# Kernel optimization log

Measured on AMD Instinct MI355X. Metric: run time of the kernel, lower is better.

Reference implementation:

```python
import jax, jax.numpy as jnp
import numpy as np

N = 100000   # nodes
IN = 128     # in_size
OUT = 64     # out_size (== out_size * layer_num_heads, heads=1)
P = 3        # meta-paths
E = 1600000  # edges per meta-path graph
HID = 32     # semantic attention hidden size


def setup_inputs() -> dict:
    key = jax.random.key(0)
    ks = jax.random.split(key, 8)
    h = jax.random.normal(ks[0], (N, IN), dtype=jnp.float32)
    edge_src = jax.random.randint(ks[1], (P, E), 0, N)
    edge_dst = jax.random.randint(ks[2], (P, E), 0, N)
    # xavier_uniform-style init for linear weights
    def xavier(k, shape):
        fan_in, fan_out = shape[0], shape[1]
        lim = np.sqrt(6.0 / (fan_in + fan_out)).astype(np.float32)
        return jax.random.uniform(k, shape, jnp.float32, -lim, lim)
    gc_w = xavier(ks[3], (IN, OUT))
    gc_b = jnp.zeros((OUT,), jnp.float32)
    sa_w1 = xavier(ks[4], (OUT, HID))
    sa_b1 = jnp.zeros((HID,), jnp.float32)
    sa_w2 = xavier(ks[5], (HID, 1))
    return {"h": h, "gc_w": gc_w, "gc_b": gc_b, "sa_w1": sa_w1,
            "sa_b1": sa_b1, "sa_w2": sa_w2,
            "edge_src": edge_src, "edge_dst": edge_dst}


def _graph_conv(h, gc_w, gc_b, src, dst):
    # DGL GraphConv, norm='both', activation=relu, allow_zero_in_degree.
    ones = jnp.ones(src.shape, h.dtype)
    out_deg = jax.ops.segment_sum(ones, src, num_segments=N)
    in_deg = jax.ops.segment_sum(ones, dst, num_segments=N)
    norm_src = jax.lax.rsqrt(jnp.maximum(out_deg, 1.0))  # [N]
    norm_dst = jax.lax.rsqrt(jnp.maximum(in_deg, 1.0))   # [N]
    # in_feats > out_feats: project first, then aggregate
    feat = (h * norm_src[:, None]) @ gc_w                # [N, OUT]
    agg = jax.ops.segment_sum(feat[src], dst, num_segments=N)  # [N, OUT]
    return jax.nn.relu(agg * norm_dst[:, None] + gc_b)


def reference(h, gc_w, gc_b, sa_w1, sa_b1, sa_w2, edge_src, edge_dst):
    # shared GraphConv applied to each meta-path graph (dropout p=0 -> identity)
    embs = [_graph_conv(h, gc_w, gc_b, edge_src[p], edge_dst[p]) for p in range(P)]
    z = jnp.stack(embs, axis=1)                          # [N, P, OUT]
    # semantic attention: small MLP -> mean over nodes -> softmax over meta-paths
    w = jnp.tanh(z @ sa_w1 + sa_b1) @ sa_w2              # [N, P, 1]
    beta = jax.nn.softmax(w.mean(axis=0), axis=0)        # [P, 1]
    out = (beta[None, :, :] * z).sum(axis=1)             # [N, OUT]
    return out, z
```

## Files before the change

kernel.cpp:

```cpp
#include <hip/hip_runtime.h>

#define NN 100000
#define IN_F 128
#define OUT_F 64
#define PP 3
#define EE 1600000
#define TOT (PP * EE)
#define HID 32
#define SEG_N (PP * NN)
#define NC1024 98
#define NCB (NC1024 * PP)
#define CAPC 19456
#define CAPS 21504
#define CHUNK 8192
#define NSX ((EE + CHUNK - 1) / CHUNK)
#define LCAP 64
#define NFB (NCB * 32)
#define WSLOTS 256

__device__ __forceinline__ unsigned short f2bf(float f) {
    unsigned u = __float_as_uint(f);
    u += 0x7FFFu + ((u >> 16) & 1u);
    return (unsigned short)(u >> 16);
}
__device__ __forceinline__ float bf2f(unsigned short b) {
    return __uint_as_float((unsigned)b << 16);
}
__device__ __forceinline__ float tanh_fast(float x) {
    float ax = fabsf(x);
    float e = __expf(-2.f * ax);
    float t = (1.f - e) / (1.f + e);
    return copysignf(t, x);
}

__global__ void scatter_coarse(const int* __restrict__ src, const int* __restrict__ dst,
                               unsigned* __restrict__ gcur_d, unsigned* __restrict__ gcur_s,
                               unsigned* __restrict__ gbuf_d, unsigned short* __restrict__ gbuf_s) {
    __shared__ unsigned cnt_d[4][NC1024], cnt_s[4][NC1024];
    __shared__ unsigned base_d[NC1024], base_s[NC1024];
    int tid = threadIdx.x;
    int wv = tid >> 6;
    int p = blockIdx.y;
    for (int i = tid; i < 4 * NC1024; i += 256) { cnt_d[i / NC1024][i % NC1024] = 0u; cnt_s[i / NC1024][i % NC1024] = 0u; }
    __syncthreads();
    int e0 = blockIdx.x * CHUNK;
    const int* sp = src + (size_t)p * EE;
    const int* dp = dst + (size_t)p * EE;
    for (int i = 0; i < CHUNK / 256; ++i) {
        int e = e0 + i * 256 + tid;
        if (e < EE) {
            atomicAdd(&cnt_d[wv][dp[e] >> 10], 1u);
            atomicAdd(&cnt_s[wv][sp[e] >> 10], 1u);
        }
    }
    __syncthreads();
    for (int i = tid; i < NC1024; i += 256) {
        unsigned c0 = cnt_d[0][i], c1 = cnt_d[1][i], c2 = cnt_d[2][i], c3 = cnt_d[3][i];
        unsigned tt = c0 + c1 + c2 + c3;
        unsigned base = tt ? atomicAdd(&gcur_d[i * PP + p], (tt + 15u) & ~15u) : 0u;
        base_d[i] = base;
        cnt_d[0][i] = base; cnt_d[1][i] = base + c0;
        cnt_d[2][i] = base + c0 + c1; cnt_d[3][i] = base + c0 + c1 + c2;
        c0 = cnt_s[0][i]; c1 = cnt_s[1][i]; c2 = cnt_s[2][i]; c3 = cnt_s[3][i];
        tt = c0 + c1 + c2 + c3;
        base = tt ? atomicAdd(&gcur_s[i * PP + p], (tt + 31u) & ~31u) : 0u;
        base_s[i] = base;
        cnt_s[0][i] = base; cnt_s[1][i] = base + c0;
        cnt_s[2][i] = base + c0 + c1; cnt_s[3][i] = base + c0 + c1 + c2;
    }
    __syncthreads();
    for (int i = 0; i < CHUNK / 256; ++i) {
        int e = e0 + i * 256 + tid;
        if (e < EE) {
            int s = sp[e], d = dp[e];
            unsigned pd = atomicAdd(&cnt_d[wv][d >> 10], 1u);
            unsigned ps = atomicAdd(&cnt_s[wv][s >> 10], 1u);
            if (pd < CAPC) gbuf_d[(size_t)((d >> 10) * PP + p) * CAPC + pd] = (unsigned)s | ((unsigned)(d & 1023) << 17);
            if (ps < CAPS) gbuf_s[(size_t)((s >> 10) * PP + p) * CAPS + ps] = (unsigned short)(s & 1023);
        }
    }
    __syncthreads();
    for (int i = tid; i < NC1024; i += 256) {
        unsigned base = base_d[i];
        unsigned tt = cnt_d[3][i] - base;
        unsigned padded = (tt + 15u) & ~15u;
        for (unsigned k = tt; k < padded; ++k)
            if (base + k < CAPC) gbuf_d[(size_t)(i * PP + p) * CAPC + base + k] = 0xFFFFFFFFu;
        base = base_s[i];
        tt = cnt_s[3][i] - base;
        padded = (tt + 31u) & ~31u;
        for (unsigned k = tt; k < padded; ++k)
            if (base + k < CAPS) gbuf_s[(size_t)(i * PP + p) * CAPS + base + k] = 0xFFFFu;
    }
}

__global__ void src_hist(const unsigned* __restrict__ gcur_s, const unsigned short* __restrict__ gbuf_s,
                         float* __restrict__ nsrc) {
    __shared__ unsigned hist[4][1024];
    int tid = threadIdx.x;
    int wv = tid >> 6;
    for (int i = tid; i < 4 * 1024; i += 256) hist[i >> 10][i & 1023] = 0u;
    __syncthreads();
    int c = blockIdx.x;
    int blk = c / PP, p = c - blk * PP;
    unsigned cnt = gcur_s[c]; if (cnt > CAPS) cnt = CAPS;
    const unsigned short* gb = gbuf_s + (size_t)c * CAPS;
    for (unsigned j = tid; j < cnt; j += 256) {
        unsigned v = gb[j];
        if (v <= 1023u) atomicAdd(&hist[wv][v], 1u);
    }
    __syncthreads();
    for (int i = tid; i < 1024; i += 256) {
        int n = blk * 1024 + i;
        unsigned hv = hist[0][i] + hist[1][i] + hist[2][i] + hist[3][i];
        if (n < NN) nsrc[p * NN + n] = rsqrtf(fmaxf((float)hv, 1.f));
    }
}

__global__ void __launch_bounds__(256) proj_fused(const float* __restrict__ h,
                                                  const float* __restrict__ gc_w,
                                                  const float* __restrict__ nsrc,
                                                  unsigned short* __restrict__ t0,
                                                  unsigned short* __restrict__ t1,
                                                  unsigned short* __restrict__ t2) {
    __shared__ float w_lds[IN_F * OUT_F];
    __shared__ float h_lds[32 * IN_F];
    int tid = threadIdx.x;
    for (int i = tid; i < IN_F * OUT_F / 4; i += 256)
        ((float4*)w_lds)[i] = ((const float4*)gc_w)[i];
    size_t r0 = (size_t)blockIdx.x * 32;
    for (int i = tid; i < 32 * IN_F / 4; i += 256)
        ((float4*)h_lds)[i] = ((const float4*)(h + r0 * IN_F))[i];
    __syncthreads();
    int wave = tid >> 6, lane = tid & 63;
    float acc[8] = {0.f, 0.f, 0.f, 0.f, 0.f, 0.f, 0.f, 0.f};
    for (int k = 0; k < IN_F; k += 4) {
        float w0 = w_lds[k * OUT_F + lane];
        float w1 = w_lds[(k + 1) * OUT_F + lane];
        float w2 = w_lds[(k + 2) * OUT_F + lane];
        float w3 = w_lds[(k + 3) * OUT_F + lane];
#pragma unroll
        for (int r = 0; r < 8; ++r) {
            float4 hv = *(const float4*)&h_lds[(wave * 8 + r) * IN_F + k];
            acc[r] = fmaf(hv.x, w0, fmaf(hv.y, w1, fmaf(hv.z, w2, fmaf(hv.w, w3, acc[r]))));
        }
    }
#pragma unroll
    for (int r = 0; r < 8; ++r) {
        size_t n = r0 + wave * 8 + r;
        float a = acc[r];
        t0[n * OUT_F + lane] = f2bf(a * nsrc[n]);
        t1[n * OUT_F + lane] = f2bf(a * nsrc[NN + n]);
        t2[n * OUT_F + lane] = f2bf(a * nsrc[2 * NN + n]);
    }
}

__global__ void fine_split(const unsigned* __restrict__ gcur_d, unsigned* __restrict__ gbuf_d,
                           unsigned* __restrict__ foff, unsigned* __restrict__ fcnt) {
    __shared__ unsigned stage[CAPC];
    __shared__ unsigned hist[4][32], pre[32], cur[4][32];
    int c = blockIdx.x;
    int tid = threadIdx.x;
    int wv = tid >> 6;
    if (tid < 32) { hist[0][tid] = 0u; hist[1][tid] = 0u; hist[2][tid] = 0u; hist[3][tid] = 0u; }
    __syncthreads();
    unsigned cnt = gcur_d[c]; if (cnt > CAPC) cnt = CAPC;
    unsigned* gb = gbuf_d + (size_t)c * CAPC;
    for (unsigned j = tid; j < cnt; j += 256) {
        unsigned v = gb[j];
        stage[j] = v;
        if (v != 0xFFFFFFFFu) atomicAdd(&hist[wv][v >> 22], 1u);
    }
    __syncthreads();
    if (tid == 0) {
        unsigned a = 0;
        for (int i = 0; i < 32; ++i) {
            pre[i] = a;
            a += hist[0][i] + hist[1][i] + hist[2][i] + hist[3][i];
        }
    }
    __syncthreads();
    if (tid < 32) {
        unsigned a = pre[tid];
        cur[0][tid] = a; a += hist[0][tid];
        cur[1][tid] = a; a += hist[1][tid];
        cur[2][tid] = a; a += hist[2][tid];
        cur[3][tid] = a; a += hist[3][tid];
        foff[c * 32 + tid] = (unsigned)c * CAPC + pre[tid];
        fcnt[c * 32 + tid] = a - pre[tid];
    }
    __syncthreads();
    for (unsigned j = tid; j < cnt; j += 256) {
        unsigned v = stage[j];
        if (v == 0xFFFFFFFFu) continue;
        unsigned pos = atomicAdd(&cur[wv][v >> 22], 1u);
        gb[pos] = v & 0x3FFFFFu;
    }
}

__global__ void __launch_bounds__(256, 8)
gather3d(const unsigned* __restrict__ foff, const unsigned* __restrict__ fcnt,
         const unsigned* __restrict__ gbuf_f,
         const unsigned short* __restrict__ t0, const unsigned short* __restrict__ t1,
         const unsigned short* __restrict__ t2,
         const float* __restrict__ gc_b, const float* __restrict__ sa_w1,
         const float* __restrict__ sa_b1, const float* __restrict__ sa_w2,
         float* __restrict__ zbuf, float* __restrict__ wsum) {
    __shared__ unsigned lists[32 * LCAP];
    __shared__ unsigned lcnt[32];
    __shared__ float zsh[4][OUT_F];
    int tid = threadIdx.x;
    int lane = tid & 63, wave = tid >> 6;
    int j = lane & 31, half = lane >> 5;
    unsigned w1p[16];
#pragma unroll
    for (int q = 0; q < 16; ++q) {
        float a = sa_w1[(half * 32 + 2 * q) * HID + j];
        float b = sa_w1[(half * 32 + 2 * q + 1) * HID + j];
        w1p[q] = (unsigned)f2bf(a) | ((unsigned)f2bf(b) << 16);
    }
    float b1r = sa_b1[j];
    float w2r = sa_w2[j];
    float bsr = gc_b[lane];
    if (tid < 32) lcnt[tid] = 0u;
    __syncthreads();

    int f = blockIdx.x;
    int c = f >> 5, sub = f & 31;
    int blk = c / PP, p = c - blk * PP;
    const unsigned short* tp = (p == 0) ? t0 : (p == 1) ? t1 : t2;
    unsigned base = foff[f];
    unsigned cnt = fcnt[f];
    for (unsigned i = tid; i < cnt; i += 256) {
        unsigned v = gbuf_f[base + i];
        unsigned node = (v >> 17) & 31;
        unsigned sl = atomicAdd(&lcnt[node], 1u);
        if (sl < LCAP) lists[node * LCAP + sl] = v;
    }
    __syncthreads();

    int nbase = blk * 1024 + sub * 32;
    float logacc = 0.f;
    for (int k = 0; k < 8; ++k) {
        int node = wave * 8 + k;
        int n = nbase + node;
        if (n >= NN) continue;
        unsigned ind = lcnt[node];
        unsigned c2 = ind < LCAP ? ind : LCAP;
        unsigned pl = lists[node * LCAP + lane];
        float acc = 0.f;
        unsigned i = 0;
        for (; i + 4 <= c2; i += 4) {
            unsigned a0 = (unsigned)__builtin_amdgcn_readlane((int)pl, (int)i);
            unsigned a1 = (unsigned)__builtin_amdgcn_readlane((int)pl, (int)i + 1);
            unsigned a2 = (unsigned)__builtin_amdgcn_readlane((int)pl, (int)i + 2);
            unsigned a3 = (unsigned)__builtin_amdgcn_readlane((int)pl, (int)i + 3);
            float p0 = bf2f(tp[(size_t)(a0 & 0x1FFFFu) * OUT_F + lane]);
            float p1 = bf2f(tp[(size_t)(a1 & 0x1FFFFu) * OUT_F + lane]);
            float p2 = bf2f(tp[(size_t)(a2 & 0x1FFFFu) * OUT_F + lane]);
            float p3 = bf2f(tp[(size_t)(a3 & 0x1FFFFu) * OUT_F + lane]);
            acc += (p0 + p1) + (p2 + p3);
        }
        for (; i < c2; ++i) {
            unsigned a0 = (unsigned)__builtin_amdgcn_readlane((int)pl, (int)i);
            acc += bf2f(tp[(size_t)(a0 & 0x1FFFFu) * OUT_F + lane]);
        }
        float ndv = rsqrtf(fmaxf((float)ind, 1.f));
        float zv = fmaxf(fmaf(acc, ndv, bsr), 0.f);
        zbuf[((size_t)n * PP + p) * OUT_F + lane] = zv;
        zsh[wave][lane] = zv;
        float hp = 0.f;
        const float4* zrow = (const float4*)&zsh[wave][half * 32];
#pragma unroll
        for (int q = 0; q < 8; ++q) {
            float4 zq = zrow[q];
            unsigned u0 = w1p[2 * q], u1 = w1p[2 * q + 1];
            hp = fmaf(zq.x, __uint_as_float(u0 << 16), hp);
            hp = fmaf(zq.y, __uint_as_float(u0 & 0xFFFF0000u), hp);
            hp = fmaf(zq.z, __uint_as_float(u1 << 16), hp);
            hp = fmaf(zq.w, __uint_as_float(u1 & 0xFFFF0000u), hp);
        }
        hp += __shfl_xor(hp, 32);
        logacc += tanh_fast(hp + b1r) * w2r;
    }
#pragma unroll
    for (int off = 1; off < 64; off <<= 1) logacc += __shfl_xor(logacc, off);
    if (lane == 0) atomicAdd(&wsum[(blockIdx.x & (WSLOTS - 1)) * PP + p], logacc * 0.5f);
}

__global__ void beta_kernel(const float* __restrict__ wsum, float* __restrict__ beta) {
    if (threadIdx.x == 0) {
        float m[PP] = {0.f, 0.f, 0.f};
        for (int i = 0; i < WSLOTS; ++i)
            for (int p = 0; p < PP; ++p) m[p] += wsum[i * PP + p];
        float mx = -1e30f;
        for (int p = 0; p < PP; ++p) { m[p] *= (1.0f / NN); mx = fmaxf(mx, m[p]); }
        float e[PP], s = 0.f;
        for (int p = 0; p < PP; ++p) { e[p] = expf(m[p] - mx); s += e[p]; }
        for (int p = 0; p < PP; ++p) beta[p] = e[p] / s;
    }
}

__global__ void out_kernel(const float* __restrict__ zbuf, const float* __restrict__ beta,
                           float* __restrict__ out) {
    int t = blockIdx.x * 256 + threadIdx.x;
    if (t >= NN * (OUT_F / 4)) return;
    int n = t >> 4;
    int q = t & 15;
    float b0 = beta[0], b1 = beta[1], b2 = beta[2];
    const float4 v0 = ((const float4*)(zbuf + ((size_t)n * PP + 0) * OUT_F))[q];
    const float4 v1 = ((const float4*)(zbuf + ((size_t)n * PP + 1) * OUT_F))[q];
    const float4 v2 = ((const float4*)(zbuf + ((size_t)n * PP + 2) * OUT_F))[q];
    float4 r;
    r.x = b0 * v0.x + b1 * v1.x + b2 * v2.x;
    r.y = b0 * v0.y + b1 * v1.y + b2 * v2.y;
    r.z = b0 * v0.z + b1 * v1.z + b2 * v2.z;
    r.w = b0 * v0.w + b1 * v1.w + b2 * v2.w;
    ((float4*)out)[t] = r;
}

extern "C" void kernel_launch(void* const* d_in, const int* in_sizes, int n_in,
                              void* d_out, int out_size, void* d_ws, size_t ws_size,
                              hipStream_t stream) {
    const float* h     = (const float*)d_in[0];
    const float* gc_w  = (const float*)d_in[1];
    const float* gc_b  = (const float*)d_in[2];
    const float* sa_w1 = (const float*)d_in[3];
    const float* sa_b1 = (const float*)d_in[4];
    const float* sa_w2 = (const float*)d_in[5];
    const int* esrc    = (const int*)d_in[6];
    const int* edst    = (const int*)d_in[7];

    float* out  = (float*)d_out;
    float* zbuf = out + (size_t)NN * OUT_F;
    unsigned short* t0 = (unsigned short*)out;
    unsigned short* t1 = t0 + (size_t)NN * OUT_F;

    char* ws = (char*)d_ws;
    const size_t OFF_GBD  = 0;
    const size_t OFF_GBS  = 22900000;
    const size_t OFF_T2   = 22900000;
    const size_t OFF_NSRC = 35800000;
    const size_t OFF_FOFF = 37100000;
    const size_t OFF_FCNT = 37150000;
    const size_t OFF_GCD  = 37200000;
    const size_t OFF_GCS  = 37210000;
    const size_t OFF_WSUM = 37220000;
    const size_t OFF_BETA = 37230000;

    unsigned* gbuf_d       = (unsigned*)(ws + OFF_GBD);
    unsigned short* gbuf_s = (unsigned short*)(ws + OFF_GBS);
    unsigned short* t2     = (unsigned short*)(ws + OFF_T2);
    float* nsrc            = (float*)(ws + OFF_NSRC);
    unsigned* foff         = (unsigned*)(ws + OFF_FOFF);
    unsigned* fcnt         = (unsigned*)(ws + OFF_FCNT);
    unsigned* gcur_d       = (unsigned*)(ws + OFF_GCD);
    unsigned* gcur_s       = (unsigned*)(ws + OFF_GCS);
    float* wsum            = (float*)(ws + OFF_WSUM);
    float* beta            = (float*)(ws + OFF_BETA);

    hipMemsetAsync(gcur_d, 0, NCB * sizeof(unsigned), stream);
    hipMemsetAsync(gcur_s, 0, NCB * sizeof(unsigned), stream);
    hipMemsetAsync(wsum, 0, WSLOTS * PP * sizeof(float), stream);

    scatter_coarse<<<dim3(NSX, PP), 256, 0, stream>>>(esrc, edst, gcur_d, gcur_s, gbuf_d, gbuf_s);
    src_hist<<<NCB, 256, 0, stream>>>(gcur_s, gbuf_s, nsrc);
    proj_fused<<<NN / 32, 256, 0, stream>>>(h, gc_w, nsrc, t0, t1, t2);
    fine_split<<<NCB, 256, 0, stream>>>(gcur_d, gbuf_d, foff, fcnt);
    gather3d<<<NFB, 256, 0, stream>>>(foff, fcnt, gbuf_d, t0, t1, t2,
                                      gc_b, sa_w1, sa_b1, sa_w2, zbuf, wsum);
    beta_kernel<<<1, 64, 0, stream>>>(wsum, beta);
    out_kernel<<<(NN * (OUT_F / 4) + 255) / 256, 256, 0, stream>>>(zbuf, beta, out);
}
```

Baseline: 416.0 us.

## Split coarse scatter into two kernels that sort edges locally in shared memory

```diff
diff --git a/kernel.cpp b/kernel.cpp
--- a/kernel.cpp
+++ b/kernel.cpp
@@ -33,64 +33,120 @@
     return copysignf(t, x);
 }
 
-__global__ void scatter_coarse(const int* __restrict__ src, const int* __restrict__ dst,
-                               unsigned* __restrict__ gcur_d, unsigned* __restrict__ gcur_s,
-                               unsigned* __restrict__ gbuf_d, unsigned short* __restrict__ gbuf_s) {
-    __shared__ unsigned cnt_d[4][NC1024], cnt_s[4][NC1024];
-    __shared__ unsigned base_d[NC1024], base_s[NC1024];
-    int tid = threadIdx.x;
-    int wv = tid >> 6;
+__global__ void scatter_sortd(const int* __restrict__ src, const int* __restrict__ dst,
+                              unsigned* __restrict__ gcur_d, unsigned* __restrict__ gbuf_d) {
+    __shared__ unsigned sorted[CHUNK];
+    __shared__ unsigned hist4[4][NC1024];
+    __shared__ unsigned pre[NC1024 + 1];
+    __shared__ unsigned wcur[4][NC1024];
+    __shared__ unsigned gbase[NC1024];
+    int tid = threadIdx.x, wv = tid >> 6;
     int p = blockIdx.y;
-    for (int i = tid; i < 4 * NC1024; i += 256) { cnt_d[i / NC1024][i % NC1024] = 0u; cnt_s[i / NC1024][i % NC1024] = 0u; }
+    for (int i = tid; i < 4 * NC1024; i += 256) hist4[i / NC1024][i % NC1024] = 0u;
     __syncthreads();
     int e0 = blockIdx.x * CHUNK;
     const int* sp = src + (size_t)p * EE;
     const int* dp = dst + (size_t)p * EE;
     for (int i = 0; i < CHUNK / 256; ++i) {
         int e = e0 + i * 256 + tid;
-        if (e < EE) {
-            atomicAdd(&cnt_d[wv][dp[e] >> 10], 1u);
-            atomicAdd(&cnt_s[wv][sp[e] >> 10], 1u);
-        }
-    }
-    __syncthreads();
-    for (int i = tid; i < NC1024; i += 256) {
-        unsigned c0 = cnt_d[0][i], c1 = cnt_d[1][i], c2 = cnt_d[2][i], c3 = cnt_d[3][i];
-        unsigned tt = c0 + c1 + c2 + c3;
-        unsigned base = tt ? atomicAdd(&gcur_d[i * PP + p], (tt + 15u) & ~15u) : 0u;
-        base_d[i] = base;
-        cnt_d[0][i] = base; cnt_d[1][i] = base + c0;
-        cnt_d[2][i] = base + c0 + c1; cnt_d[3][i] = base + c0 + c1 + c2;
-        c0 = cnt_s[0][i]; c1 = cnt_s[1][i]; c2 = cnt_s[2][i]; c3 = cnt_s[3][i];
-        tt = c0 + c1 + c2 + c3;
-        base = tt ? atomicAdd(&gcur_s[i * PP + p], (tt + 31u) & ~31u) : 0u;
-        base_s[i] = base;
-        cnt_s[0][i] = base; cnt_s[1][i] = base + c0;
-        cnt_s[2][i] = base + c0 + c1; cnt_s[3][i] = base + c0 + c1 + c2;
+        if (e < EE) atomicAdd(&hist4[wv][dp[e] >> 10], 1u);
+    }
+    __syncthreads();
+    if (tid == 0) {
+        unsigned a = 0;
+        for (int b = 0; b < NC1024; ++b) {
+            pre[b] = a;
+            a += hist4[0][b] + hist4[1][b] + hist4[2][b] + hist4[3][b];
+        }
+        pre[NC1024] = a;
+    }
+    __syncthreads();
+    if (tid < NC1024) {
+        unsigned a = pre[tid];
+        wcur[0][tid] = a; a += hist4[0][tid];
+        wcur[1][tid] = a; a += hist4[1][tid];
+        wcur[2][tid] = a; a += hist4[2][tid];
+        wcur[3][tid] = a; a += hist4[3][tid];
+        unsigned tt = a - pre[tid];
+        gbase[tid] = tt ? atomicAdd(&gcur_d[tid * PP + p], (tt + 15u) & ~15u) : 0u;
     }
     __syncthreads();
     for (int i = 0; i < CHUNK / 256; ++i) {
         int e = e0 + i * 256 + tid;
         if (e < EE) {
             int s = sp[e], d = dp[e];
-            unsigned pd = atomicAdd(&cnt_d[wv][d >> 10], 1u);
-            unsigned ps = atomicAdd(&cnt_s[wv][s >> 10], 1u);
-            if (pd < CAPC) gbuf_d[(size_t)((d >> 10) * PP + p) * CAPC + pd] = (unsigned)s | ((unsigned)(d & 1023) << 17);
-            if (ps < CAPS) gbuf_s[(size_t)((s >> 10) * PP + p) * CAPS + ps] = (unsigned short)(s & 1023);
-        }
-    }
-    __syncthreads();
-    for (int i = tid; i < NC1024; i += 256) {
-        unsigned base = base_d[i];
-        unsigned tt = cnt_d[3][i] - base;
-        unsigned padded = (tt + 15u) & ~15u;
-        for (unsigned k = tt; k < padded; ++k)
-            if (base + k < CAPC) gbuf_d[(size_t)(i * PP + p) * CAPC + base + k] = 0xFFFFFFFFu;
-        base = base_s[i];
-        tt = cnt_s[3][i] - base;
-        padded = (tt + 31u) & ~31u;
-        for (unsigned k = tt; k < padded; ++k)
-            if (base + k < CAPS) gbuf_s[(size_t)(i * PP + p) * CAPS + base + k] = 0xFFFFu;
+            unsigned pos = atomicAdd(&wcur[wv][(unsigned)d >> 10], 1u);
+            sorted[pos] = (unsigned)s | ((unsigned)(d & 1023) << 17);
+        }
+    }
+    __syncthreads();
+    for (int b = 0; b < NC1024; ++b) {
+        unsigned st = pre[b], len = pre[b + 1] - st;
+        if (!len) continue;
+        unsigned padded = (len + 15u) & ~15u;
+        unsigned gb = gbase[b];
+        size_t gout = (size_t)(b * PP + p) * CAPC;
+        for (unsigned j = tid; j < padded; j += 256)
+            if (gb + j < CAPC)
+                gbuf_d[gout + gb + j] = (j < len) ? sorted[st + j] : 0xFFFFFFFFu;
+    }
+}
+
+__global__ void scatter_sorts(const int* __restrict__ src,
+                              unsigned* __restrict__ gcur_s, unsigned short* __restrict__ gbuf_s) {
+    __shared__ unsigned short sorted[CHUNK];
+    __shared__ unsigned hist4[4][NC1024];
+    __shared__ unsigned pre[NC1024 + 1];
+    __shared__ unsigned wcur[4][NC1024];
+    __shared__ unsigned gbase[NC1024];
+    int tid = threadIdx.x, wv = tid >> 6;
+    int p = blockIdx.y;
+    for (int i = tid; i < 4 * NC1024; i += 256) hist4[i / NC1024][i % NC1024] = 0u;
+    __syncthreads();
+    int e0 = blockIdx.x * CHUNK;
+    const int* sp = src + (size_t)p * EE;
+    for (int i = 0; i < CHUNK / 256; ++i) {
+        int e = e0 + i * 256 + tid;
+        if (e < EE) atomicAdd(&hist4[wv][sp[e] >> 10], 1u);
+    }
+    __syncthreads();
+    if (tid == 0) {
+        unsigned a = 0;
+        for (int b = 0; b < NC1024; ++b) {
+            pre[b] = a;
+            a += hist4[0][b] + hist4[1][b] + hist4[2][b] + hist4[3][b];
+        }
+        pre[NC1024] = a;
+    }
+    __syncthreads();
+    if (tid < NC1024) {
+        unsigned a = pre[tid];
+        wcur[0][tid] = a; a += hist4[0][tid];
+        wcur[1][tid] = a; a += hist4[1][tid];
+        wcur[2][tid] = a; a += hist4[2][tid];
+        wcur[3][tid] = a; a += hist4[3][tid];
+        unsigned tt = a - pre[tid];
+        gbase[tid] = tt ? atomicAdd(&gcur_s[tid * PP + p], (tt + 31u) & ~31u) : 0u;
+    }
+    __syncthreads();
+    for (int i = 0; i < CHUNK / 256; ++i) {
+        int e = e0 + i * 256 + tid;
+        if (e < EE) {
+            int s = sp[e];
+            unsigned pos = atomicAdd(&wcur[wv][(unsigned)s >> 10], 1u);
+            sorted[pos] = (unsigned short)(s & 1023);
+        }
+    }
+    __syncthreads();
+    for (int b = 0; b < NC1024; ++b) {
+        unsigned st = pre[b], len = pre[b + 1] - st;
+        if (!len) continue;
+        unsigned padded = (len + 31u) & ~31u;
+        unsigned gb = gbase[b];
+        size_t gout = (size_t)(b * PP + p) * CAPS;
+        for (unsigned j = tid; j < padded; j += 256)
+            if (gb + j < CAPS)
+                gbuf_s[gout + gb + j] = (j < len) ? sorted[st + j] : (unsigned short)0xFFFFu;
     }
 }
 
@@ -363,7 +419,8 @@
     hipMemsetAsync(gcur_s, 0, NCB * sizeof(unsigned), stream);
     hipMemsetAsync(wsum, 0, WSLOTS * PP * sizeof(float), stream);
 
-    scatter_coarse<<<dim3(NSX, PP), 256, 0, stream>>>(esrc, edst, gcur_d, gcur_s, gbuf_d, gbuf_s);
+    scatter_sortd<<<dim3(NSX, PP), 256, 0, stream>>>(esrc, edst, gcur_d, gbuf_d);
+    scatter_sorts<<<dim3(NSX, PP), 256, 0, stream>>>(esrc, gcur_s, gbuf_s);
     src_hist<<<NCB, 256, 0, stream>>>(gcur_s, gbuf_s, nsrc);
     proj_fused<<<NN / 32, 256, 0, stream>>>(h, gc_w, nsrc, t0, t1, t2);
     fine_split<<<NCB, 256, 0, stream>>>(gcur_d, gbuf_d, foff, fcnt);
```

Result: faster. 404.1 us (-2.9%).
